# Performance work log

Measured on AMD Instinct MI355X. Metric: run time of the kernel, lower is better.

The kernel has to match this reference:

```python
import jax, jax.numpy as jnp
import numpy as np

N_NODES = 50000
N_EDGES = 800000
N_GRAPHS = 64
EPS = 1e-12


def setup_inputs() -> dict:
    key = jax.random.key(0)
    ks = jax.random.split(key, 8)
    x = jax.random.normal(ks[0], (N_NODES, 128), dtype=jnp.float32)
    edge_index = jax.random.randint(ks[1], (2, N_EDGES), 0, N_NODES, dtype=jnp.int64)
    batch = jnp.sort(jax.random.randint(ks[2], (N_NODES,), 0, N_GRAPHS, dtype=jnp.int64))
    W1 = jax.random.normal(ks[3], (128, 64), dtype=jnp.float32) * 0.1
    W2 = jax.random.normal(ks[4], (64, 64), dtype=jnp.float32) * 0.1
    W3 = jax.random.normal(ks[5], (64, 64), dtype=jnp.float32) * 0.1
    Wl = jax.random.normal(ks[6], (128, 32), dtype=jnp.float32) * 0.1
    return {
        'x': x, 'edge_index': edge_index, 'batch': batch,
        'W1': W1, 'b1': jnp.zeros((64,), jnp.float32),
        'W2': W2, 'b2': jnp.zeros((64,), jnp.float32),
        'W3': W3, 'b3': jnpp if False else jnp.zeros((64,), jnp.float32),
        'Wl': Wl, 'bl': jnp.zeros((32,), jnp.float32),
    }


def _gcn_conv(h, W, b, src, dst, dinv, enorm, n):
    # PyG GCNConv: D^-1/2 (A+I) D^-1/2 (h W) + b, self-loops included analytically
    hw = h @ W
    agg = jax.ops.segment_sum(hw[src] * enorm[:, None], dst, num_segments=n)
    agg = agg + (dinv * dinv)[:, None] * hw  # self-loop term
    return agg + b


def _norm_relu(h):
    # F.normalize(p=2, dim=1) then relu
    nrm = jnp.sqrt(jnp.sum(h * h, axis=1, keepdims=True))
    return jax.nn.relu(h / jnp.maximum(nrm, EPS))


def reference(x, edge_index, batch, W1, b1, W2, b2, W3, b3, Wl, bl):
    n = x.shape[0]
    src, dst = edge_index[0], edge_index[1]
    # degree with self-loops (counts incoming edges at target, +1 for self-loop)
    deg = jax.ops.segment_sum(jnp.ones((src.shape[0],), x.dtype), dst, num_segments=n) + 1.0
    dinv = 1.0 / jnp.sqrt(deg)
    enorm = dinv[src] * dinv[dst]

    h = _norm_relu(_gcn_conv(x, W1, b1, src, dst, dinv, enorm, n))
    h = _norm_relu(_gcn_conv(h, W2, b2, src, dst, dinv, enorm, n))
    h = _norm_relu(_gcn_conv(h, W3, b3, src, dst, dinv, enorm, n))

    counts = jax.ops.segment_sum(jnp.ones((n,), x.dtype), batch, num_segments=N_GRAPHS)
    x_mean = jax.ops.segment_sum(h, batch, num_segments=N_GRAPHS) / jnp.maximum(counts, 1.0)[:, None]
    x_max = jax.ops.segment_max(h, batch, num_segments=N_GRAPHS)
    x_max = jnp.where(counts[:, None] > 0, x_max, 0.0)  # guard empty graphs

    pooled = jnp.concatenate([x_mean, x_max], axis=-1)  # [B, 2*hidden]
    return pooled @ Wl + bl
```

## Files before the change

### kernel.cpp

```cpp
#include <hip/hip_runtime.h>
#include <hip/hip_bf16.h>

#define N_NODES 50000
#define N_EDGES 800000
#define N_GRAPHS 64
#define HID 64
#define SCAN_NB 196
#define FILL_RANGES 8
#define RANGE_SIZE ((N_NODES + FILL_RANGES - 1) / FILL_RANGES)

static inline size_t align256(size_t x) { return (x + 255) & ~(size_t)255; }

typedef __attribute__((ext_vector_type(8))) short short8v;
typedef __attribute__((ext_vector_type(4))) float f32x4;

__device__ __forceinline__ unsigned short f2bf(float f) {
    unsigned int u = __float_as_uint(f);
    unsigned int r = (u + 0x7fffu + ((u >> 16) & 1u)) >> 16;
    return (unsigned short)r;
}
__device__ __forceinline__ float bf2f(unsigned short h) {
    return __uint_as_float(((unsigned int)h) << 16);
}

__global__ void zero2(int* __restrict__ a, int na, int* __restrict__ b, int nb) {
    int i = blockIdx.x * blockDim.x + threadIdx.x;
    if (i < na) a[i] = 0;
    else if (i < na + nb) b[i - na] = 0;
}

__global__ void deg_kernel(const int* __restrict__ ei, int* __restrict__ cnt) {
    int e = blockIdx.x * blockDim.x + threadIdx.x;
    if (e < N_EDGES) atomicAdd(&cnt[ei[N_EDGES + e]], 1);
}

__global__ __launch_bounds__(256) void scan_a(const int* __restrict__ cnt,
                                              int* __restrict__ incl,
                                              int* __restrict__ bsum) {
    __shared__ int sd[256];
    int t = threadIdx.x;
    int i = blockIdx.x * 256 + t;
    int v = (i < N_NODES) ? cnt[i] : 0;
    sd[t] = v;
    __syncthreads();
    for (int off = 1; off < 256; off <<= 1) {
        int u = (t >= off) ? sd[t - off] : 0;
        __syncthreads();
        sd[t] += u;
        __syncthreads();
    }
    if (i < N_NODES) incl[i] = sd[t];
    if (t == 255) bsum[blockIdx.x] = sd[255];
}

__global__ __launch_bounds__(384) void scan_b_gstart(const int* __restrict__ bsum,
                                                     int* __restrict__ boff,
                                                     const int* __restrict__ batch,
                                                     int* __restrict__ gstart) {
    __shared__ int sd[256];
    int t = threadIdx.x;
    int v = 0;
    if (t < 256) {
        v = (t < SCAN_NB) ? bsum[t] : 0;
        sd[t] = v;
    }
    __syncthreads();
    for (int off = 1; off < 256; off <<= 1) {
        int u = (t < 256 && t >= off) ? sd[t - off] : 0;
        __syncthreads();
        if (t < 256) sd[t] += u;
        __syncthreads();
    }
    if (t < SCAN_NB) boff[t] = sd[t] - v;
    if (t >= 256 && t - 256 <= N_GRAPHS) {
        int g = t - 256;
        int lo = 0, hi = N_NODES;
        while (lo < hi) {
            int mid = (lo + hi) >> 1;
            if (batch[mid] < g) lo = mid + 1; else hi = mid;
        }
        gstart[g] = lo;
    }
}

__global__ void scan_c(const int* __restrict__ cnt, const int* __restrict__ incl,
                       const int* __restrict__ boff, int* __restrict__ row_ptr,
                       int* __restrict__ fill_ptr, float* __restrict__ dinv) {
    int i = blockIdx.x * blockDim.x + threadIdx.x;
    if (i < N_NODES) {
        int c = cnt[i];
        int run = boff[i >> 8] + incl[i];
        row_ptr[i + 1] = run;
        fill_ptr[i] = run - c;
        dinv[i] = rsqrtf((float)c + 1.0f);
        if (i == 0) row_ptr[0] = 0;
    }
}

__global__ __launch_bounds__(256) void fill_kernel(const int* __restrict__ ei,
                                                   int* __restrict__ fill_ptr,
                                                   int* __restrict__ csr_src) {
    int r = blockIdx.x & (FILL_RANGES - 1);
    int e = (blockIdx.x >> 3) * 256 + threadIdx.x;
    if (e >= N_EDGES) return;
    int dst = ei[N_EDGES + e];
    int lo = r * RANGE_SIZE;
    if (dst >= lo && dst < lo + RANGE_SIZE) {
        int src = ei[e];
        int pos = atomicAdd(&fill_ptr[dst], 1);
        csr_src[pos] = src;
    }
}

template <int K>
__global__ __launch_bounds__(256) void mfma_matmul(const float* __restrict__ h,
                                                   const float* __restrict__ W,
                                                   const float* __restrict__ dinv,
                                                   unsigned short* __restrict__ hw2) {
    constexpr int NSTEP = K / 32;
    __shared__ unsigned short sWH[NSTEP * 4 * 64 * 8];
    __shared__ unsigned short sWL[NSTEP * 4 * 64 * 8];
    int tid = threadIdx.x;
    int r0 = blockIdx.x * 64;

#pragma unroll 1
    for (int ent = tid; ent < NSTEP * 4 * 64; ent += 256) {
        int lane_e = ent & 63;
        int c = (ent >> 6) & 3;
        int step = ent >> 8;
        int kb = step * 32 + (lane_e >> 4) * 8;
        int n = c * 16 + (lane_e & 15);
#pragma unroll
        for (int j = 0; j < 8; ++j) {
            float f = W[(kb + j) * 64 + n];
            unsigned short hi = f2bf(f);
            sWH[ent * 8 + j] = hi;
            sWL[ent * 8 + j] = f2bf(f - bf2f(hi));
        }
    }
    __syncthreads();

    int lane = tid & 63;
    int wid = tid >> 6;
    int arow = min(r0 + wid * 16 + (lane & 15), N_NODES - 1);
    const float* ap = h + (size_t)arow * K;
    int klane = (lane >> 4) * 8;

    f32x4 acc[4];
#pragma unroll
    for (int c = 0; c < 4; ++c) acc[c] = (f32x4){0.f, 0.f, 0.f, 0.f};

#pragma unroll 1
    for (int step = 0; step < NSTEP; ++step) {
        int kb = step * 32 + klane;
        float4 f0 = *(const float4*)&ap[kb];
        float4 f1 = *(const float4*)&ap[kb + 4];
        float fv[8] = {f0.x, f0.y, f0.z, f0.w, f1.x, f1.y, f1.z, f1.w};
        short8v ahi, alo;
#pragma unroll
        for (int j = 0; j < 8; ++j) {
            unsigned short hi = f2bf(fv[j]);
            ahi[j] = (short)hi;
            alo[j] = (short)f2bf(fv[j] - bf2f(hi));
        }
#pragma unroll
        for (int c = 0; c < 4; ++c) {
            short8v bh = *(const short8v*)&sWH[((step * 4 + c) * 64 + lane) * 8];
            short8v bl = *(const short8v*)&sWL[((step * 4 + c) * 64 + lane) * 8];
            acc[c] = __builtin_amdgcn_mfma_f32_16x16x32_bf16(ahi, bh, acc[c], 0, 0, 0);
            acc[c] = __builtin_amdgcn_mfma_f32_16x16x32_bf16(alo, bh, acc[c], 0, 0, 0);
            acc[c] = __builtin_amdgcn_mfma_f32_16x16x32_bf16(ahi, bl, acc[c], 0, 0, 0);
        }
    }

    int rb = r0 + wid * 16 + (lane >> 4) * 4;
#pragma unroll
    for (int j = 0; j < 4; ++j) {
        int row = rb + j;
        if (row < N_NODES) {
            float dv = dinv[row];
#pragma unroll
            for (int c = 0; c < 4; ++c) {
                hw2[(size_t)row * 64 + c * 16 + (lane & 15)] = f2bf(dv * acc[c][j]);
            }
        }
    }
}

template <bool POOL>
__global__ __launch_bounds__(256) void agg_kernel(const unsigned short* __restrict__ hw2,
                                                  const int* __restrict__ row_ptr,
                                                  const int* __restrict__ csr_src,
                                                  const float* __restrict__ dinv,
                                                  const float* __restrict__ b,
                                                  float* __restrict__ hout,
                                                  const int* __restrict__ batch,
                                                  float* __restrict__ gsum,
                                                  float* __restrict__ gmax) {
    __shared__ float sh[4][64];
    int tid = threadIdx.x;
    int node = blockIdx.x * 4 + (tid >> 6);
    int lane = tid & 63;
    int grp = lane >> 3;
    int gl  = lane & 7;
    int s = row_ptr[node], e = row_ptr[node + 1];

    float acc[8] = {0.f, 0.f, 0.f, 0.f, 0.f, 0.f, 0.f, 0.f};
    for (int base = s; base < e; base += 64) {
        int nE = min(64, e - base);
        int msrc = (lane < nE) ? csr_src[base + lane] : 0;
#pragma unroll 2
        for (int i = 0; i < nE; i += 8) {
            int myi = i + grp;
            int src = __shfl(msrc, myi, 64);
            if (myi < nE) {
                short8v v = *(const short8v*)&hw2[(size_t)src * 64 + gl * 8];
#pragma unroll
                for (int j = 0; j < 8; ++j) acc[j] += bf2f((unsigned short)v[j]);
            }
        }
    }
#pragma unroll
    for (int off = 8; off <= 32; off <<= 1) {
#pragma unroll
        for (int j = 0; j < 8; ++j) acc[j] += __shfl_xor(acc[j], off, 64);
    }
    short8v sv = *(const short8v*)&hw2[(size_t)node * 64 + gl * 8];
#pragma unroll
    for (int j = 0; j < 8; ++j) acc[j] += bf2f((unsigned short)sv[j]);

    float di = dinv[node];
    float4 b0 = *(const float4*)&b[gl * 8];
    float4 b1 = *(const float4*)&b[gl * 8 + 4];
    float val[8];
    val[0] = di * acc[0] + b0.x;
    val[1] = di * acc[1] + b0.y;
    val[2] = di * acc[2] + b0.z;
    val[3] = di * acc[3] + b0.w;
    val[4] = di * acc[4] + b1.x;
    val[5] = di * acc[5] + b1.y;
    val[6] = di * acc[6] + b1.z;
    val[7] = di * acc[7] + b1.w;

    float sq = 0.f;
#pragma unroll
    for (int j = 0; j < 8; ++j) sq += val[j] * val[j];
#pragma unroll
    for (int off = 1; off <= 4; off <<= 1) sq += __shfl_xor(sq, off, 64);
    float inv = 1.0f / fmaxf(sqrtf(sq), 1e-12f);

    if (POOL) {
        if (grp == 0) {
            float4 r0, r1;
            r0.x = fmaxf(val[0] * inv, 0.f);
            r0.y = fmaxf(val[1] * inv, 0.f);
            r0.z = fmaxf(val[2] * inv, 0.f);
            r0.w = fmaxf(val[3] * inv, 0.f);
            r1.x = fmaxf(val[4] * inv, 0.f);
            r1.y = fmaxf(val[5] * inv, 0.f);
            r1.z = fmaxf(val[6] * inv, 0.f);
            r1.w = fmaxf(val[7] * inv, 0.f);
            *(float4*)&sh[tid >> 6][gl * 8] = r0;
            *(float4*)&sh[tid >> 6][gl * 8 + 4] = r1;
        }
        __syncthreads();
        if (tid < 64) {
            int nb = blockIdx.x * 4;
            int gcur = batch[nb];
            float runsum = 0.f, runmax = 0.f;
#pragma unroll
            for (int w = 0; w < 4; ++w) {
                int g = batch[nb + w];
                if (g != gcur) {
                    atomicAdd(&gsum[gcur * 64 + tid], runsum);
                    atomicMax((int*)&gmax[gcur * 64 + tid], __float_as_int(runmax));
                    runsum = 0.f; runmax = 0.f; gcur = g;
                }
                float v = sh[w][tid];
                runsum += v;
                runmax = fmaxf(runmax, v);
            }
            atomicAdd(&gsum[gcur * 64 + tid], runsum);
            atomicMax((int*)&gmax[gcur * 64 + tid], __float_as_int(runmax));
        }
    } else {
        if (grp == 0) {
            float4 r0, r1;
            r0.x = fmaxf(val[0] * inv, 0.f);
            r0.y = fmaxf(val[1] * inv, 0.f);
            r0.z = fmaxf(val[2] * inv, 0.f);
            r0.w = fmaxf(val[3] * inv, 0.f);
            r1.x = fmaxf(val[4] * inv, 0.f);
            r1.y = fmaxf(val[5] * inv, 0.f);
            r1.z = fmaxf(val[6] * inv, 0.f);
            r1.w = fmaxf(val[7] * inv, 0.f);
            *(float4*)&hout[(size_t)node * 64 + gl * 8] = r0;
            *(float4*)&hout[(size_t)node * 64 + gl * 8 + 4] = r1;
        }
    }
}

__global__ __launch_bounds__(128) void linear_kernel(const float* __restrict__ gsum,
                                                     const float* __restrict__ gmax,
                                                     const int* __restrict__ gstart,
                                                     const float* __restrict__ Wl,
                                                     const float* __restrict__ bl,
                                                     float* __restrict__ out) {
    int g = blockIdx.x;
    __shared__ float pooled[128];
    int t = threadIdx.x;
    if (t < 64) {
        int cnt = gstart[g + 1] - gstart[g];
        pooled[t] = gsum[g * 64 + t] / fmaxf((float)cnt, 1.0f);
    } else {
        pooled[t] = gmax[g * 64 + (t - 64)];
    }
    __syncthreads();
    if (t < 32) {
        float acc = bl[t];
#pragma unroll 8
        for (int k = 0; k < 128; ++k) acc += pooled[k] * Wl[k * 32 + t];
        out[g * 32 + t] = acc;
    }
}

extern "C" void kernel_launch(void* const* d_in, const int* in_sizes, int n_in,
                              void* d_out, int out_size, void* d_ws, size_t ws_size,
                              hipStream_t stream) {
    const float* x        = (const float*)d_in[0];
    const int*   ei       = (const int*)d_in[1];
    const int*   batch    = (const int*)d_in[2];
    const float* W1       = (const float*)d_in[3];
    const float* b1       = (const float*)d_in[4];
    const float* W2       = (const float*)d_in[5];
    const float* b2       = (const float*)d_in[6];
    const float* W3       = (const float*)d_in[7];
    const float* b3       = (const float*)d_in[8];
    const float* Wl       = (const float*)d_in[9];
    const float* bl       = (const float*)d_in[10];
    float* out = (float*)d_out;

    char* ws = (char*)d_ws;
    int*   cnt      = (int*)ws;                 ws += align256((size_t)N_NODES * 4);
    int*   incl     = (int*)ws;                 ws += align256((size_t)N_NODES * 4);
    int*   bsum     = (int*)ws;                 ws += align256((size_t)SCAN_NB * 4);
    int*   boff     = (int*)ws;                 ws += align256((size_t)SCAN_NB * 4);
    int*   row_ptr  = (int*)ws;                 ws += align256((size_t)(N_NODES + 1) * 4);
    int*   fill_ptr = (int*)ws;                 ws += align256((size_t)N_NODES * 4);
    float* dinv     = (float*)ws;               ws += align256((size_t)N_NODES * 4);
    int*   gstart   = (int*)ws;                 ws += align256((size_t)(N_GRAPHS + 1) * 4);
    float* gsum     = (float*)ws;               ws += align256((size_t)N_GRAPHS * 64 * 4);
    float* gmax     = (float*)ws;               ws += align256((size_t)N_GRAPHS * 64 * 4);
    int*   csr_src  = (int*)ws;                 ws += align256((size_t)N_EDGES * 4);
    unsigned short* hwb = (unsigned short*)ws;  ws += align256((size_t)N_NODES * 64 * 2);
    float* h1       = (float*)ws;               ws += align256((size_t)N_NODES * 64 * 4);
    float* h2       = (float*)ws;               ws += align256((size_t)N_NODES * 64 * 4);

    hipLaunchKernelGGL(zero2, dim3((N_NODES + 2 * N_GRAPHS * 64 + 255) / 256), dim3(256), 0,
                       stream, cnt, N_NODES, (int*)gsum, 2 * N_GRAPHS * 64);
    hipLaunchKernelGGL(deg_kernel, dim3((N_EDGES + 255) / 256), dim3(256), 0, stream, ei, cnt);
    hipLaunchKernelGGL(scan_a, dim3(SCAN_NB), dim3(256), 0, stream, cnt, incl, bsum);
    hipLaunchKernelGGL(scan_b_gstart, dim3(1), dim3(384), 0, stream, bsum, boff, batch, gstart);
    hipLaunchKernelGGL(scan_c, dim3(SCAN_NB), dim3(256), 0, stream,
                       cnt, incl, boff, row_ptr, fill_ptr, dinv);
    hipLaunchKernelGGL(fill_kernel,
                       dim3(FILL_RANGES * ((N_EDGES + 255) / 256)), dim3(256), 0, stream,
                       ei, fill_ptr, csr_src);

    const int mm_grid = (N_NODES + 63) / 64;
    const int agg_grid = N_NODES / 4;

    hipLaunchKernelGGL((mfma_matmul<128>), dim3(mm_grid), dim3(256), 0, stream, x, W1, dinv, hwb);
    hipLaunchKernelGGL((agg_kernel<false>), dim3(agg_grid), dim3(256), 0, stream,
                       hwb, row_ptr, csr_src, dinv, b1, h1, batch, gsum, gmax);
    hipLaunchKernelGGL((mfma_matmul<64>), dim3(mm_grid), dim3(256), 0, stream, h1, W2, dinv, hwb);
    hipLaunchKernelGGL((agg_kernel<false>), dim3(agg_grid), dim3(256), 0, stream,
                       hwb, row_ptr, csr_src, dinv, b2, h2, batch, gsum, gmax);
    hipLaunchKernelGGL((mfma_matmul<64>), dim3(mm_grid), dim3(256), 0, stream, h2, W3, dinv, hwb);
    hipLaunchKernelGGL((agg_kernel<true>), dim3(agg_grid), dim3(256), 0, stream,
                       hwb, row_ptr, csr_src, dinv, b3, (float*)nullptr, batch, gsum, gmax);

    hipLaunchKernelGGL(linear_kernel, dim3(N_GRAPHS), dim3(128), 0, stream,
                       gsum, gmax, gstart, Wl, bl, out);
}
```

Baseline: 212.9 us.

## Fuse CSR fill with first-layer MFMA matmul and unroll aggregation gather loop

The edge-to-CSR fill and the first layer's bf16-split MFMA matmul become one launch. The first 782 blocks do the matmul and the remaining blocks do the fill, so the two independent pieces of work can overlap and one launch is dropped. The fill blocks now carry the matmul's shared-memory allocation, which may lower their occupancy. Separately, the aggregation inner loop is fully unrolled and issues its loads unconditionally, using the node's own row for out-of-range slots, so more loads can be in flight at the cost of some redundant reads.

Result: faster. 207.7 us (-2.4%).

```diff
diff --git a/kernel.cpp b/kernel.cpp
--- a/kernel.cpp
+++ b/kernel.cpp
@@ -8,6 +8,8 @@
 #define SCAN_NB 196
 #define FILL_RANGES 8
 #define RANGE_SIZE ((N_NODES + FILL_RANGES - 1) / FILL_RANGES)
+#define MM1_BLOCKS ((N_NODES + 63) / 64)
+#define FILL_BLOCKS (FILL_RANGES * ((N_EDGES + 255) / 256))
 
 static inline size_t align256(size_t x) { return (x + 255) & ~(size_t)255; }
 
@@ -97,18 +99,96 @@
     }
 }
 
-__global__ __launch_bounds__(256) void fill_kernel(const int* __restrict__ ei,
-                                                   int* __restrict__ fill_ptr,
-                                                   int* __restrict__ csr_src) {
-    int r = blockIdx.x & (FILL_RANGES - 1);
-    int e = (blockIdx.x >> 3) * 256 + threadIdx.x;
-    if (e >= N_EDGES) return;
-    int dst = ei[N_EDGES + e];
-    int lo = r * RANGE_SIZE;
-    if (dst >= lo && dst < lo + RANGE_SIZE) {
-        int src = ei[e];
-        int pos = atomicAdd(&fill_ptr[dst], 1);
-        csr_src[pos] = src;
+__global__ __launch_bounds__(256) void fill_mm1_kernel(const int* __restrict__ ei,
+                                                       int* __restrict__ fill_ptr,
+                                                       int* __restrict__ csr_src,
+                                                       const float* __restrict__ h,
+                                                       const float* __restrict__ W,
+                                                       const float* __restrict__ dinv,
+                                                       unsigned short* __restrict__ hw2) {
+    constexpr int K = 128;
+    constexpr int NSTEP = K / 32;
+    __shared__ unsigned short sWH[NSTEP * 4 * 64 * 8];
+    __shared__ unsigned short sWL[NSTEP * 4 * 64 * 8];
+    int tid = threadIdx.x;
+
+    if (blockIdx.x >= MM1_BLOCKS) {
+        int fb = blockIdx.x - MM1_BLOCKS;
+        int r = fb & (FILL_RANGES - 1);
+        int e = (fb >> 3) * 256 + tid;
+        if (e >= N_EDGES) return;
+        int dst = ei[N_EDGES + e];
+        int lo = r * RANGE_SIZE;
+        if (dst >= lo && dst < lo + RANGE_SIZE) {
+            int src = ei[e];
+            int pos = atomicAdd(&fill_ptr[dst], 1);
+            csr_src[pos] = src;
+        }
+        return;
+    }
+
+    int r0 = blockIdx.x * 64;
+#pragma unroll 1
+    for (int ent = tid; ent < NSTEP * 4 * 64; ent += 256) {
+        int lane_e = ent & 63;
+        int c = (ent >> 6) & 3;
+        int step = ent >> 8;
+        int kb = step * 32 + (lane_e >> 4) * 8;
+        int n = c * 16 + (lane_e & 15);
+#pragma unroll
+        for (int j = 0; j < 8; ++j) {
+            float f = W[(kb + j) * 64 + n];
+            unsigned short hi = f2bf(f);
+            sWH[ent * 8 + j] = hi;
+            sWL[ent * 8 + j] = f2bf(f - bf2f(hi));
+        }
+    }
+    __syncthreads();
+
+    int lane = tid & 63;
+    int wid = tid >> 6;
+    int arow = min(r0 + wid * 16 + (lane & 15), N_NODES - 1);
+    const float* ap = h + (size_t)arow * K;
+    int klane = (lane >> 4) * 8;
+
+    f32x4 acc[4];
+#pragma unroll
+    for (int c = 0; c < 4; ++c) acc[c] = (f32x4){0.f, 0.f, 0.f, 0.f};
+
+#pragma unroll 1
+    for (int step = 0; step < NSTEP; ++step) {
+        int kb = step * 32 + klane;
+        float4 f0 = *(const float4*)&ap[kb];
+        float4 f1 = *(const float4*)&ap[kb + 4];
+        float fv[8] = {f0.x, f0.y, f0.z, f0.w, f1.x, f1.y, f1.z, f1.w};
+        short8v ahi, alo;
+#pragma unroll
+        for (int j = 0; j < 8; ++j) {
+            unsigned short hi = f2bf(fv[j]);
+            ahi[j] = (short)hi;
+            alo[j] = (short)f2bf(fv[j] - bf2f(hi));
+        }
+#pragma unroll
+        for (int c = 0; c < 4; ++c) {
+            short8v bh = *(const short8v*)&sWH[((step * 4 + c) * 64 + lane) * 8];
+            short8v bl = *(const short8v*)&sWL[((step * 4 + c) * 64 + lane) * 8];
+            acc[c] = __builtin_amdgcn_mfma_f32_16x16x32_bf16(ahi, bh, acc[c], 0, 0, 0);
+            acc[c] = __builtin_amdgcn_mfma_f32_16x16x32_bf16(alo, bh, acc[c], 0, 0, 0);
+            acc[c] = __builtin_amdgcn_mfma_f32_16x16x32_bf16(ahi, bl, acc[c], 0, 0, 0);
+        }
+    }
+
+    int rb = r0 + wid * 16 + (lane >> 4) * 4;
+#pragma unroll
+    for (int j = 0; j < 4; ++j) {
+        int row = rb + j;
+        if (row < N_NODES) {
+            float dv = dinv[row];
+#pragma unroll
+            for (int c = 0; c < 4; ++c) {
+                hw2[(size_t)row * 64 + c * 16 + (lane & 15)] = f2bf(dv * acc[c][j]);
+            }
+        }
     }
 }
 
@@ -209,12 +289,16 @@
     for (int base = s; base < e; base += 64) {
         int nE = min(64, e - base);
         int msrc = (lane < nE) ? csr_src[base + lane] : 0;
-#pragma unroll 2
-        for (int i = 0; i < nE; i += 8) {
+#pragma unroll
+        for (int rr = 0; rr < 8; ++rr) {
+            int i = rr * 8;
+            if (i >= nE) break;
             int myi = i + grp;
             int src = __shfl(msrc, myi, 64);
-            if (myi < nE) {
-                short8v v = *(const short8v*)&hw2[(size_t)src * 64 + gl * 8];
+            bool ok = myi < nE;
+            int srcx = ok ? src : node;
+            short8v v = *(const short8v*)&hw2[(size_t)srcx * 64 + gl * 8];
+            if (ok) {
 #pragma unroll
                 for (int j = 0; j < 8; ++j) acc[j] += bf2f((unsigned short)v[j]);
             }
@@ -363,14 +447,13 @@
     hipLaunchKernelGGL(scan_b_gstart, dim3(1), dim3(384), 0, stream, bsum, boff, batch, gstart);
     hipLaunchKernelGGL(scan_c, dim3(SCAN_NB), dim3(256), 0, stream,
                        cnt, incl, boff, row_ptr, fill_ptr, dinv);
-    hipLaunchKernelGGL(fill_kernel,
-                       dim3(FILL_RANGES * ((N_EDGES + 255) / 256)), dim3(256), 0, stream,
-                       ei, fill_ptr, csr_src);
 
     const int mm_grid = (N_NODES + 63) / 64;
     const int agg_grid = N_NODES / 4;
 
-    hipLaunchKernelGGL((mfma_matmul<128>), dim3(mm_grid), dim3(256), 0, stream, x, W1, dinv, hwb);
+    hipLaunchKernelGGL(fill_mm1_kernel, dim3(MM1_BLOCKS + FILL_BLOCKS), dim3(256), 0, stream,
+                       ei, fill_ptr, csr_src, x, W1, dinv, hwb);
+
     hipLaunchKernelGGL((agg_kernel<false>), dim3(agg_grid), dim3(256), 0, stream,
                        hwb, row_ptr, csr_src, dinv, b1, h1, batch, gsum, gmax);
     hipLaunchKernelGGL((mfma_matmul<64>), dim3(mm_grid), dim3(256), 0, stream, h1, W2, dinv, hwb);
```
